# Kernel optimization log

Hardware: AMD Instinct MI355X
Metric: run time of the kernel (lower is better)

## Reference

```python
import jax, jax.numpy as jnp
import numpy as np

NEG = -1.0e30  # finite stand-in for -inf (NaN-safe under autodiff)


def rnnt_loss_mean(logits, ys, ylen):
    # logits: (B, T, U+1, V); ys: (B, U) int labels; ylen: (B,) label lengths.
    # blank index = 0; per the original forward, xlen == T for every batch element.
    lp = jax.nn.log_softmax(logits, axis=-1)
    lp_blank = lp[..., 0]  # (B, T, U1)
    # lp_label[b, t, u] = lp[b, t, u, ys[b, u]]  for u < U
    lp_label = jnp.take_along_axis(
        lp[:, :, :-1, :], ys[:, None, :, None].astype(jnp.int32), axis=3
    )[..., 0]  # (B, T, U)
    B, T, U1 = lp_blank.shape
    # emit[b, t, u] = lp_label[b, t, u-1], with emit[..., 0] = -inf
    emit = jnp.concatenate([jnp.full((B, T, 1), NEG, lp.dtype), lp_label], axis=2)
    # alpha[0, u] = sum_{k<u} lp_label[b, 0, k]
    row0 = jnp.concatenate(
        [jnp.zeros((B, 1), lp.dtype), jnp.cumsum(lp_label[:, 0, :], axis=1)], axis=1
    )  # (B, U1)

    def u_step(carry, au_eu):
        a_u, e_u = au_eu  # each (B,)
        new = jnp.logaddexp(a_u, carry + e_u)
        return new, new

    def t_step(prev_row, inp):
        blank_prev, emit_t = inp  # each (B, U1)
        a = prev_row + blank_prev  # horizontal (time) move
        init = jnp.full((B,), NEG, lp.dtype)
        _, new_row = jax.lax.scan(u_step, init, (a.T, emit_t.T))  # (U1, B)
        return new_row.T, None

    last_row, _ = jax.lax.scan(
        t_step,
        row0,
        (jnp.swapaxes(lp_blank[:, :-1, :], 0, 1), jnp.swapaxes(emit[:, 1:, :], 0, 1)),
    )  # (B, U1) = alpha[T-1, :]
    yl = ylen[:, None].astype(jnp.int32)
    alpha_end = jnp.take_along_axis(last_row, yl, axis=1)[:, 0]
    blank_end = jnp.take_along_axis(lp_blank[:, T - 1, :], yl, axis=1)[:, 0]
    return jnp.mean(-(alpha_end + blank_end))


def setup_inputs():
    B, T, U, H, V = 8, 200, 50, 320, 1024
    key = jax.random.key(0)
    ks = jax.random.split(key, 12)
    s = np.float32(1.0 / np.sqrt(H))
    return {
        "encoder_output": jax.random.normal(ks[0], (B, T, H), jnp.float32),
        "prediction_output": jax.random.normal(ks[1], (B, U + 1, H), jnp.float32),
        "xs": jax.random.normal(ks[2], (B, T, 80), jnp.float32),  # unused by forward
        "xlen": jnp.full((B,), T, jnp.int32),  # overwritten to T in original code
        "ys": jax.random.randint(ks[3], (B, U), 1, V, dtype=jnp.int32),
        "ylen": jax.random.randint(ks[4], (B,), 1, U + 1, dtype=jnp.int32),
        "W_enc": jax.random.normal(ks[5], (H, H), jnp.float32) * s,
        "b_enc": jnp.zeros((H,), jnp.float32),
        "W_pred": jax.random.normal(ks[6], (H, H), jnp.float32) * s,
        "b_pred": jnp.zeros((H,), jnp.float32),
        "W_ff_enc": jax.random.normal(ks[7], (H, V), jnp.float32) * s,
        "W_ff_pred": jax.random.normal(ks[8], (H, V), jnp.float32) * s,
        "b_ff": jnp.zeros((V,), jnp.float32),
    }


def reference(encoder_output, prediction_output, xs, xlen, ys, ylen,
              W_enc, b_enc, W_pred, b_pred, W_ff_enc, W_ff_pred, b_ff):
    # linear_enc / linear_pred commute with the broadcast-expand, so apply them first.
    enc_proj = encoder_output @ W_enc + b_enc        # (B, T, H)
    pred_proj = prediction_output @ W_pred + b_pred  # (B, U1, H)
    # cat + linear_feed_forward == split-weight matmuls summed over the broadcast.
    enc_part = enc_proj @ W_ff_enc    # (B, T, V)
    pred_part = pred_proj @ W_ff_pred  # (B, U1, V)
    logits = enc_part[:, :, None, :] + pred_part[:, None, :, :] + b_ff  # (B, T, U1, V)
    loss = rnnt_loss_mean(logits, ys, ylen)
    return loss, logits
```

## Files before the change

kernel.cpp:

```cpp
#include <hip/hip_runtime.h>
#include <hip/hip_bf16.h>
#include <cstddef>

#define Bdim 8
#define Tdim 200
#define Udim 50
#define U1dim 51
#define Hdim 320
#define Vdim 1024
#define NEGV -1.0e30f

using short8 = __attribute__((ext_vector_type(8))) short;
using f32x4  = __attribute__((ext_vector_type(4))) float;

static __device__ __forceinline__ ushort f2bf(float x) {
    __hip_bfloat16 h = __float2bfloat16(x);
    return *reinterpret_cast<ushort*>(&h);
}

__global__ __launch_bounds__(256) void cvt_bf16(
    const float* __restrict__ in, ushort* __restrict__ out, int n4)
{
    int i = blockIdx.x * 256 + threadIdx.x;
    if (i >= n4) return;
    float4 v = ((const float4*)in)[i];
    ushort4 o;
    o.x = f2bf(v.x); o.y = f2bf(v.y); o.z = f2bf(v.z); o.w = f2bf(v.w);
    ((ushort4*)out)[i] = o;
}

__global__ __launch_bounds__(256) void transpose_cvt(
    const float* __restrict__ W, ushort* __restrict__ Wt, int K, int N)
{
    __shared__ float tile[32][33];
    const int tx = threadIdx.x & 31, ty = threadIdx.x >> 5;
    const int n0 = blockIdx.x * 32, k0 = blockIdx.y * 32;
    #pragma unroll
    for (int i = 0; i < 4; ++i)
        tile[ty + i * 8][tx] = W[(size_t)(k0 + ty + i * 8) * N + n0 + tx];
    __syncthreads();
    #pragma unroll
    for (int i = 0; i < 4; ++i)
        Wt[(size_t)(n0 + ty + i * 8) * K + k0 + tx] = f2bf(tile[tx][ty + i * 8]);
}

template <bool OUT_BF16>
__global__ __launch_bounds__(256) void gemm_mfma(
    const ushort* __restrict__ A, const ushort* __restrict__ Bt,
    const float* __restrict__ bias, void* __restrict__ Cout,
    int M, int N, int K)
{
    __shared__ short As[64][40];
    __shared__ short Bs[64][40];
    const int tid = threadIdx.x;
    const int m0 = blockIdx.y * 64;
    const int n0 = blockIdx.x * 64;

    const int srow = tid >> 2;
    const int skc  = (tid & 3) * 8;

    const int lane = tid & 63;
    const int wave = tid >> 6;
    const int wr = wave >> 1, wc = wave & 1;
    const int lrow = lane & 15;
    const int kg = (lane >> 4) * 8;

    f32x4 acc[2][2] = {};

    for (int k0 = 0; k0 < K; k0 += 32) {
        int4 av = make_int4(0, 0, 0, 0);
        if (m0 + srow < M)
            av = *(const int4*)&A[(size_t)(m0 + srow) * K + k0 + skc];
        *(int4*)&As[srow][skc] = av;
        int4 bv = *(const int4*)&Bt[(size_t)(n0 + srow) * K + k0 + skc];
        *(int4*)&Bs[srow][skc] = bv;
        __syncthreads();

        short8 a0 = *(const short8*)&As[wr * 32 + lrow][kg];
        short8 a1 = *(const short8*)&As[wr * 32 + 16 + lrow][kg];
        short8 b0 = *(const short8*)&Bs[wc * 32 + lrow][kg];
        short8 b1 = *(const short8*)&Bs[wc * 32 + 16 + lrow][kg];
        acc[0][0] = __builtin_amdgcn_mfma_f32_16x16x32_bf16(a0, b0, acc[0][0], 0, 0, 0);
        acc[0][1] = __builtin_amdgcn_mfma_f32_16x16x32_bf16(a0, b1, acc[0][1], 0, 0, 0);
        acc[1][0] = __builtin_amdgcn_mfma_f32_16x16x32_bf16(a1, b0, acc[1][0], 0, 0, 0);
        acc[1][1] = __builtin_amdgcn_mfma_f32_16x16x32_bf16(a1, b1, acc[1][1], 0, 0, 0);
        __syncthreads();
    }

    #pragma unroll
    for (int fm = 0; fm < 2; ++fm) {
        #pragma unroll
        for (int fn = 0; fn < 2; ++fn) {
            int col = n0 + wc * 32 + fn * 16 + lrow;
            int r0 = m0 + wr * 32 + fm * 16 + (lane >> 4) * 4;
            float bv = bias ? bias[col] : 0.f;
            #pragma unroll
            for (int r = 0; r < 4; ++r) {
                int row = r0 + r;
                if (row < M) {
                    float val = acc[fm][fn][r] + bv;
                    if (OUT_BF16)
                        ((ushort*)Cout)[(size_t)row * N + col] = f2bf(val);
                    else
                        ((float*)Cout)[(size_t)row * N + col] = val;
                }
            }
        }
    }
}

__global__ __launch_bounds__(256) void joint_lse(
    const float* __restrict__ enc_part, const float* __restrict__ pred_part,
    const int* __restrict__ ys, float* __restrict__ out,
    float* __restrict__ lp_blank, float* __restrict__ lp_label)
{
    const int bt = blockIdx.x;
    const int b = bt / Tdim;
    const int tid = threadIdx.x;
    __shared__ float E[Vdim];
    *(float4*)&E[tid * 4] = *(const float4*)&enc_part[(size_t)bt * Vdim + tid * 4];
    __syncthreads();

    const int lane = tid & 63;
    const int wave = tid >> 6;
    float* logits = out + 1;

    for (int u = wave; u < U1dim; u += 4) {
        const float* P = pred_part + (size_t)(b * U1dim + u) * Vdim;
        float* Lrow = logits + ((size_t)bt * U1dim + u) * Vdim;
        float l[16];
        float m = -3.0e38f;
        #pragma unroll
        for (int k = 0; k < 16; ++k) {
            int v = k * 64 + lane;
            float x = E[v] + P[v];
            l[k] = x;
            Lrow[v] = x;
            m = fmaxf(m, x);
        }
        #pragma unroll
        for (int off = 32; off >= 1; off >>= 1) m = fmaxf(m, __shfl_xor(m, off));
        float s = 0.f;
        #pragma unroll
        for (int k = 0; k < 16; ++k) s += __expf(l[k] - m);
        #pragma unroll
        for (int off = 32; off >= 1; off >>= 1) s += __shfl_xor(s, off);
        float lse = m + __logf(s);

        int vlab = (u < Udim) ? ys[b * Udim + u] : 0;
        int ksel = vlab >> 6;
        int lsel = vlab & 63;
        float cand = 0.f;
        #pragma unroll
        for (int k = 0; k < 16; ++k) if (k == ksel) cand = l[k];
        float lab = __shfl(cand, lsel);
        float l0 = __shfl(l[0], 0);

        if (lane == 0) {
            lp_blank[(size_t)bt * U1dim + u] = l0 - lse;
            if (u < Udim) lp_label[(size_t)bt * Udim + u] = lab - lse;
        }
    }
}

__global__ __launch_bounds__(256) void alpha_kernel(
    const float* __restrict__ lp_blank, const float* __restrict__ lp_label,
    const int* __restrict__ ylen, float* __restrict__ loss_part)
{
    __shared__ float s_bl[U1dim * Tdim];
    __shared__ float s_lab[Udim * Tdim];
    const int b = blockIdx.x;
    const int tid = threadIdx.x;
    const float* gb = lp_blank + (size_t)b * Tdim * U1dim;
    const float* gl = lp_label + (size_t)b * Tdim * Udim;
    for (int i = tid; i < Tdim * U1dim; i += 256) {
        int t = i / U1dim, u = i % U1dim;
        s_bl[u * Tdim + t] = gb[i];
    }
    for (int i = tid; i < Tdim * Udim; i += 256) {
        int t = i / Udim, u = i % Udim;
        s_lab[u * Tdim + t] = gl[i];
    }
    __syncthreads();

    if (tid < 64) {
        const int u = tid;
        float cur = NEGV;
        for (int d = 0; d < Tdim + U1dim - 1; ++d) {
            float left = __shfl_up(cur, 1);
            int t = d - u;
            if (u < U1dim && t >= 0 && t < Tdim) {
                float h = (t >= 1) ? cur + s_bl[u * Tdim + (t - 1)] : NEGV;
                float g = (u >= 1) ? left + s_lab[(u - 1) * Tdim + t] : NEGV;
                float mx = fmaxf(h, g);
                float nv = mx + log1pf(__expf(-fabsf(h - g)));
                if (d == 0) nv = 0.f;
                cur = nv;
            }
        }
        const int L = ylen[b];
        if (u == L) loss_part[b] = -(cur + s_bl[L * Tdim + (Tdim - 1)]);
    }
}

__global__ void loss_mean(const float* __restrict__ loss_part, float* __restrict__ out)
{
    if (threadIdx.x == 0) {
        float s = 0.f;
        for (int i = 0; i < Bdim; ++i) s += loss_part[i];
        out[0] = s * (1.0f / Bdim);
    }
}

extern "C" void kernel_launch(void* const* d_in, const int* in_sizes, int n_in,
                              void* d_out, int out_size, void* d_ws, size_t ws_size,
                              hipStream_t stream)
{
    const float* enc      = (const float*)d_in[0];
    const float* pred     = (const float*)d_in[1];
    const int*   ys       = (const int*)d_in[4];
    const int*   ylen     = (const int*)d_in[5];
    const float* W_enc    = (const float*)d_in[6];
    const float* b_enc    = (const float*)d_in[7];
    const float* W_pred   = (const float*)d_in[8];
    const float* b_pred   = (const float*)d_in[9];
    const float* W_ff_enc = (const float*)d_in[10];
    const float* W_ff_pred= (const float*)d_in[11];
    const float* b_ff     = (const float*)d_in[12];
    float* out = (float*)d_out;
    char* ws = (char*)d_ws;

    ushort* enc_bf       = (ushort*)(ws + 0);
    ushort* pred_bf      = (ushort*)(ws + 1024000);
    float*  enc_part     = (float*) (ws + 0);
    float*  pred_part    = (float*) (ws + 6553600);
    float*  lp_blank     = (float*) (ws + 8224768);
    float*  lp_label     = (float*) (ws + 8551168);
    float*  loss_part    = (float*) (ws + 8871168);
    ushort* Wenc_t       = (ushort*)(ws + 8871200);
    ushort* Wpred_t      = (ushort*)(ws + 9076000);
    ushort* Wffe_t       = (ushort*)(ws + 9280800);
    ushort* Wffp_t       = (ushort*)(ws + 9936160);
    ushort* enc_proj_bf  = (ushort*)(ws + 10591520);
    ushort* pred_proj_bf = (ushort*)(ws + 11615520);

    dim3 blk(256);

    cvt_bf16<<<dim3(500), blk, 0, stream>>>(enc, enc_bf, 128000);
    cvt_bf16<<<dim3(128), blk, 0, stream>>>(pred, pred_bf, 32640);
    transpose_cvt<<<dim3(10, 10), blk, 0, stream>>>(W_enc,     Wenc_t, Hdim, Hdim);
    transpose_cvt<<<dim3(10, 10), blk, 0, stream>>>(W_pred,    Wpred_t, Hdim, Hdim);
    transpose_cvt<<<dim3(32, 10), blk, 0, stream>>>(W_ff_enc,  Wffe_t, Hdim, Vdim);
    transpose_cvt<<<dim3(32, 10), blk, 0, stream>>>(W_ff_pred, Wffp_t, Hdim, Vdim);

    gemm_mfma<true><<<dim3(5, 25), blk, 0, stream>>>(enc_bf, Wenc_t, b_enc, enc_proj_bf, Bdim * Tdim, Hdim, Hdim);
    gemm_mfma<true><<<dim3(5, 7), blk, 0, stream>>>(pred_bf, Wpred_t, b_pred, pred_proj_bf, Bdim * U1dim, Hdim, Hdim);
    gemm_mfma<false><<<dim3(16, 25), blk, 0, stream>>>(enc_proj_bf, Wffe_t, nullptr, enc_part, Bdim * Tdim, Vdim, Hdim);
    gemm_mfma<false><<<dim3(16, 7), blk, 0, stream>>>(pred_proj_bf, Wffp_t, b_ff, pred_part, Bdim * U1dim, Vdim, Hdim);

    joint_lse<<<dim3(Bdim * Tdim), blk, 0, stream>>>(enc_part, pred_part, ys, out, lp_blank, lp_label);
    alpha_kernel<<<dim3(Bdim), blk, 0, stream>>>(lp_blank, lp_label, ylen, loss_part);
    loss_mean<<<dim3(1), dim3(64), 0, stream>>>(loss_part, out);
}
```

Measured before the change: 243.9 us.

## Precompose projection weights and merge GEMMs, vectorize joint LSE, fold loss mean

The change multiplies W_ff by W_enc/W_pred once to form fused weights and bias vectors, turning two chained GEMMs per branch into one. Fp32 activations are converted to bf16 inside the GEMM load, which removes the separate convert and transpose kernels. Enc and pred GEMMs run in a single launch. joint_lse now loads contiguous float4 chunks per lane instead of going through shared memory, and the final mean becomes an atomicAdd in alpha_kernel. This cuts the launch count from thirteen to four and avoids intermediate buffers. In exchange, numerics change because the weights are precomposed in bf16, the float sum order becomes nondeterministic, and logits stores are unaligned because out is offset by one.

```diff
diff --git a/kernel.cpp b/kernel.cpp
--- a/kernel.cpp
+++ b/kernel.cpp
@@ -17,47 +17,54 @@
     __hip_bfloat16 h = __float2bfloat16(x);
     return *reinterpret_cast<ushort*>(&h);
 }
-
-__global__ __launch_bounds__(256) void cvt_bf16(
-    const float* __restrict__ in, ushort* __restrict__ out, int n4)
-{
-    int i = blockIdx.x * 256 + threadIdx.x;
-    if (i >= n4) return;
-    float4 v = ((const float4*)in)[i];
-    ushort4 o;
-    o.x = f2bf(v.x); o.y = f2bf(v.y); o.z = f2bf(v.z); o.w = f2bf(v.w);
-    ((ushort4*)out)[i] = o;
-}
-
-__global__ __launch_bounds__(256) void transpose_cvt(
-    const float* __restrict__ W, ushort* __restrict__ Wt, int K, int N)
-{
-    __shared__ float tile[32][33];
-    const int tx = threadIdx.x & 31, ty = threadIdx.x >> 5;
-    const int n0 = blockIdx.x * 32, k0 = blockIdx.y * 32;
-    #pragma unroll
-    for (int i = 0; i < 4; ++i)
-        tile[ty + i * 8][tx] = W[(size_t)(k0 + ty + i * 8) * N + n0 + tx];
-    __syncthreads();
-    #pragma unroll
-    for (int i = 0; i < 4; ++i)
-        Wt[(size_t)(n0 + ty + i * 8) * K + k0 + tx] = f2bf(tile[tx][ty + i * 8]);
-}
-
-template <bool OUT_BF16>
-__global__ __launch_bounds__(256) void gemm_mfma(
-    const ushort* __restrict__ A, const ushort* __restrict__ Bt,
-    const float* __restrict__ bias, void* __restrict__ Cout,
-    int M, int N, int K)
-{
+static __device__ __forceinline__ int pack2(float a, float b) {
+    return (int)f2bf(a) | ((int)f2bf(b) << 16);
+}
+
+__global__ __launch_bounds__(256) void fuse_weights(
+    const float* __restrict__ W_enc, const float* __restrict__ W_ff_enc,
+    const float* __restrict__ W_pred, const float* __restrict__ W_ff_pred,
+    const float* __restrict__ b_enc, const float* __restrict__ b_pred,
+    const float* __restrict__ b_ff,
+    ushort* __restrict__ Wfe_t, ushort* __restrict__ Wfp_t,
+    float* __restrict__ cvec, float* __restrict__ dvec)
+{
+    const int tid = threadIdx.x;
+    if (blockIdx.y == 16) {
+        if (blockIdx.x > 1) return;
+        const bool e = (blockIdx.x == 0);
+        const float* bv = e ? b_enc : b_pred;
+        const float* Wf = e ? W_ff_enc : W_ff_pred;
+        float* ovec = e ? cvec : dvec;
+        const int v = tid * 4;
+        float4 acc = make_float4(0.f, 0.f, 0.f, 0.f);
+        for (int p = 0; p < Hdim; ++p) {
+            float s = bv[p];
+            float4 w = *(const float4*)&Wf[(size_t)p * Vdim + v];
+            acc.x += s * w.x; acc.y += s * w.y; acc.z += s * w.z; acc.w += s * w.w;
+        }
+        if (e) {
+            float4 bf = *(const float4*)&b_ff[v];
+            acc.x += bf.x; acc.y += bf.y; acc.z += bf.z; acc.w += bf.w;
+        }
+        *(float4*)&ovec[v] = acc;
+        return;
+    }
+
+    const bool e = (blockIdx.x < 5);
+    const float* A  = e ? W_ff_enc : W_ff_pred;
+    const float* Bm = e ? W_enc    : W_pred;
+    ushort* Cout    = e ? Wfe_t    : Wfp_t;
+    const int n0 = (blockIdx.x % 5) * 64;
+    const int m0 = blockIdx.y * 64;
+
     __shared__ short As[64][40];
     __shared__ short Bs[64][40];
-    const int tid = threadIdx.x;
-    const int m0 = blockIdx.y * 64;
-    const int n0 = blockIdx.x * 64;
-
-    const int srow = tid >> 2;
-    const int skc  = (tid & 3) * 8;
+
+    const int ar = tid >> 3;
+    const int ac = (tid & 7) * 8;
+    const int br = tid >> 2;
+    const int bc = (tid & 3) * 8;
 
     const int lane = tid & 63;
     const int wave = tid >> 6;
@@ -67,23 +74,32 @@
 
     f32x4 acc[2][2] = {};
 
-    for (int k0 = 0; k0 < K; k0 += 32) {
-        int4 av = make_int4(0, 0, 0, 0);
-        if (m0 + srow < M)
-            av = *(const int4*)&A[(size_t)(m0 + srow) * K + k0 + skc];
-        *(int4*)&As[srow][skc] = av;
-        int4 bv = *(const int4*)&Bt[(size_t)(n0 + srow) * K + k0 + skc];
-        *(int4*)&Bs[srow][skc] = bv;
+    for (int k0 = 0; k0 < Hdim; k0 += 32) {
+        float4 a0 = *(const float4*)&A[(size_t)(k0 + ar) * Vdim + m0 + ac];
+        float4 a1 = *(const float4*)&A[(size_t)(k0 + ar) * Vdim + m0 + ac + 4];
+        As[ac + 0][ar] = (short)f2bf(a0.x);
+        As[ac + 1][ar] = (short)f2bf(a0.y);
+        As[ac + 2][ar] = (short)f2bf(a0.z);
+        As[ac + 3][ar] = (short)f2bf(a0.w);
+        As[ac + 4][ar] = (short)f2bf(a1.x);
+        As[ac + 5][ar] = (short)f2bf(a1.y);
+        As[ac + 6][ar] = (short)f2bf(a1.z);
+        As[ac + 7][ar] = (short)f2bf(a1.w);
+        float4 w0 = *(const float4*)&Bm[(size_t)(n0 + br) * Hdim + k0 + bc];
+        float4 w1 = *(const float4*)&Bm[(size_t)(n0 + br) * Hdim + k0 + bc + 4];
+        int4 bp = make_int4(pack2(w0.x, w0.y), pack2(w0.z, w0.w),
+                            pack2(w1.x, w1.y), pack2(w1.z, w1.w));
+        *(int4*)&Bs[br][bc] = bp;
         __syncthreads();
 
-        short8 a0 = *(const short8*)&As[wr * 32 + lrow][kg];
-        short8 a1 = *(const short8*)&As[wr * 32 + 16 + lrow][kg];
-        short8 b0 = *(const short8*)&Bs[wc * 32 + lrow][kg];
-        short8 b1 = *(const short8*)&Bs[wc * 32 + 16 + lrow][kg];
-        acc[0][0] = __builtin_amdgcn_mfma_f32_16x16x32_bf16(a0, b0, acc[0][0], 0, 0, 0);
-        acc[0][1] = __builtin_amdgcn_mfma_f32_16x16x32_bf16(a0, b1, acc[0][1], 0, 0, 0);
-        acc[1][0] = __builtin_amdgcn_mfma_f32_16x16x32_bf16(a1, b0, acc[1][0], 0, 0, 0);
-        acc[1][1] = __builtin_amdgcn_mfma_f32_16x16x32_bf16(a1, b1, acc[1][1], 0, 0, 0);
+        short8 fa0 = *(const short8*)&As[wr * 32 + lrow][kg];
+        short8 fa1 = *(const short8*)&As[wr * 32 + 16 + lrow][kg];
+        short8 fb0 = *(const short8*)&Bs[wc * 32 + lrow][kg];
+        short8 fb1 = *(const short8*)&Bs[wc * 32 + 16 + lrow][kg];
+        acc[0][0] = __builtin_amdgcn_mfma_f32_16x16x32_bf16(fa0, fb0, acc[0][0], 0, 0, 0);
+        acc[0][1] = __builtin_amdgcn_mfma_f32_16x16x32_bf16(fa0, fb1, acc[0][1], 0, 0, 0);
+        acc[1][0] = __builtin_amdgcn_mfma_f32_16x16x32_bf16(fa1, fb0, acc[1][0], 0, 0, 0);
+        acc[1][1] = __builtin_amdgcn_mfma_f32_16x16x32_bf16(fa1, fb1, acc[1][1], 0, 0, 0);
         __syncthreads();
     }
 
@@ -93,17 +109,77 @@
         for (int fn = 0; fn < 2; ++fn) {
             int col = n0 + wc * 32 + fn * 16 + lrow;
             int r0 = m0 + wr * 32 + fm * 16 + (lane >> 4) * 4;
-            float bv = bias ? bias[col] : 0.f;
+            #pragma unroll
+            for (int r = 0; r < 4; ++r)
+                Cout[(size_t)(r0 + r) * Hdim + col] = f2bf(acc[fm][fn][r]);
+        }
+    }
+}
+
+__global__ __launch_bounds__(256) void main_gemm(
+    const float* __restrict__ enc, const float* __restrict__ pred,
+    const ushort* __restrict__ Wfe_t, const ushort* __restrict__ Wfp_t,
+    const float* __restrict__ cvec, const float* __restrict__ dvec,
+    float* __restrict__ enc_part, float* __restrict__ pred_part)
+{
+    const bool e = (blockIdx.y < 25);
+    const float*  A    = e ? enc : pred;
+    const ushort* Bt   = e ? Wfe_t : Wfp_t;
+    const float*  bias = e ? cvec : dvec;
+    float*        C    = e ? enc_part : pred_part;
+    const int M  = e ? (Bdim * Tdim) : (Bdim * U1dim);
+    const int m0 = (e ? blockIdx.y : blockIdx.y - 25) * 64;
+    const int n0 = blockIdx.x * 64;
+
+    __shared__ short As[64][40];
+    __shared__ short Bs[64][40];
+    const int tid = threadIdx.x;
+    const int sr = tid >> 2;
+    const int sc = (tid & 3) * 8;
+
+    const int lane = tid & 63;
+    const int wave = tid >> 6;
+    const int wr = wave >> 1, wc = wave & 1;
+    const int lrow = lane & 15;
+    const int kg = (lane >> 4) * 8;
+
+    f32x4 acc[2][2] = {};
+
+    for (int k0 = 0; k0 < Hdim; k0 += 32) {
+        int4 av = make_int4(0, 0, 0, 0);
+        if (m0 + sr < M) {
+            float4 x0 = *(const float4*)&A[(size_t)(m0 + sr) * Hdim + k0 + sc];
+            float4 x1 = *(const float4*)&A[(size_t)(m0 + sr) * Hdim + k0 + sc + 4];
+            av = make_int4(pack2(x0.x, x0.y), pack2(x0.z, x0.w),
+                           pack2(x1.x, x1.y), pack2(x1.z, x1.w));
+        }
+        *(int4*)&As[sr][sc] = av;
+        *(int4*)&Bs[sr][sc] = *(const int4*)&Bt[(size_t)(n0 + sr) * Hdim + k0 + sc];
+        __syncthreads();
+
+        short8 fa0 = *(const short8*)&As[wr * 32 + lrow][kg];
+        short8 fa1 = *(const short8*)&As[wr * 32 + 16 + lrow][kg];
+        short8 fb0 = *(const short8*)&Bs[wc * 32 + lrow][kg];
+        short8 fb1 = *(const short8*)&Bs[wc * 32 + 16 + lrow][kg];
+        acc[0][0] = __builtin_amdgcn_mfma_f32_16x16x32_bf16(fa0, fb0, acc[0][0], 0, 0, 0);
+        acc[0][1] = __builtin_amdgcn_mfma_f32_16x16x32_bf16(fa0, fb1, acc[0][1], 0, 0, 0);
+        acc[1][0] = __builtin_amdgcn_mfma_f32_16x16x32_bf16(fa1, fb0, acc[1][0], 0, 0, 0);
+        acc[1][1] = __builtin_amdgcn_mfma_f32_16x16x32_bf16(fa1, fb1, acc[1][1], 0, 0, 0);
+        __syncthreads();
+    }
+
+    #pragma unroll
+    for (int fm = 0; fm < 2; ++fm) {
+        #pragma unroll
+        for (int fn = 0; fn < 2; ++fn) {
+            int col = n0 + wc * 32 + fn * 16 + lrow;
+            int r0 = m0 + wr * 32 + fm * 16 + (lane >> 4) * 4;
+            float bv = bias[col];
             #pragma unroll
             for (int r = 0; r < 4; ++r) {
                 int row = r0 + r;
-                if (row < M) {
-                    float val = acc[fm][fn][r] + bv;
-                    if (OUT_BF16)
-                        ((ushort*)Cout)[(size_t)row * N + col] = f2bf(val);
-                    else
-                        ((float*)Cout)[(size_t)row * N + col] = val;
-                }
+                if (row < M)
+                    C[(size_t)row * Vdim + col] = acc[fm][fn][r] + bv;
             }
         }
     }
@@ -117,44 +193,57 @@
     const int bt = blockIdx.x;
     const int b = bt / Tdim;
     const int tid = threadIdx.x;
-    __shared__ float E[Vdim];
-    *(float4*)&E[tid * 4] = *(const float4*)&enc_part[(size_t)bt * Vdim + tid * 4];
-    __syncthreads();
-
     const int lane = tid & 63;
     const int wave = tid >> 6;
+    if (bt == 0 && tid == 0) out[0] = 0.f;
+
+    const float* Erow = enc_part + (size_t)bt * Vdim + lane * 16;
+    float4 e0 = *(const float4*)(Erow + 0);
+    float4 e1 = *(const float4*)(Erow + 4);
+    float4 e2 = *(const float4*)(Erow + 8);
+    float4 e3 = *(const float4*)(Erow + 12);
+
     float* logits = out + 1;
 
     for (int u = wave; u < U1dim; u += 4) {
-        const float* P = pred_part + (size_t)(b * U1dim + u) * Vdim;
-        float* Lrow = logits + ((size_t)bt * U1dim + u) * Vdim;
-        float l[16];
-        float m = -3.0e38f;
-        #pragma unroll
-        for (int k = 0; k < 16; ++k) {
-            int v = k * 64 + lane;
-            float x = E[v] + P[v];
-            l[k] = x;
-            Lrow[v] = x;
-            m = fmaxf(m, x);
-        }
+        const float* P = pred_part + (size_t)(b * U1dim + u) * Vdim + lane * 16;
+        float4 p0 = *(const float4*)(P + 0);
+        float4 p1 = *(const float4*)(P + 4);
+        float4 p2 = *(const float4*)(P + 8);
+        float4 p3 = *(const float4*)(P + 12);
+        float xa[16];
+        xa[0]=e0.x+p0.x;  xa[1]=e0.y+p0.y;  xa[2]=e0.z+p0.z;  xa[3]=e0.w+p0.w;
+        xa[4]=e1.x+p1.x;  xa[5]=e1.y+p1.y;  xa[6]=e1.z+p1.z;  xa[7]=e1.w+p1.w;
+        xa[8]=e2.x+p2.x;  xa[9]=e2.y+p2.y;  xa[10]=e2.z+p2.z; xa[11]=e2.w+p2.w;
+        xa[12]=e3.x+p3.x; xa[13]=e3.y+p3.y; xa[14]=e3.z+p3.z; xa[15]=e3.w+p3.w;
+
+        float* L = logits + (size_t)bt * U1dim * Vdim + (size_t)u * Vdim + lane * 16;
+        L[0] = xa[0]; L[1] = xa[1]; L[2] = xa[2];
+        *(float4*)(L + 3)  = make_float4(xa[3],  xa[4],  xa[5],  xa[6]);
+        *(float4*)(L + 7)  = make_float4(xa[7],  xa[8],  xa[9],  xa[10]);
+        *(float4*)(L + 11) = make_float4(xa[11], xa[12], xa[13], xa[14]);
+        L[15] = xa[15];
+
+        float m = xa[0];
+        #pragma unroll
+        for (int i = 1; i < 16; ++i) m = fmaxf(m, xa[i]);
         #pragma unroll
         for (int off = 32; off >= 1; off >>= 1) m = fmaxf(m, __shfl_xor(m, off));
         float s = 0.f;
         #pragma unroll
-        for (int k = 0; k < 16; ++k) s += __expf(l[k] - m);
+        for (int i = 0; i < 16; ++i) s += __expf(xa[i] - m);
         #pragma unroll
         for (int off = 32; off >= 1; off >>= 1) s += __shfl_xor(s, off);
         float lse = m + __logf(s);
 
         int vlab = (u < Udim) ? ys[b * Udim + u] : 0;
-        int ksel = vlab >> 6;
-        int lsel = vlab & 63;
-        float cand = 0.f;
-        #pragma unroll
-        for (int k = 0; k < 16; ++k) if (k == ksel) cand = l[k];
-        float lab = __shfl(cand, lsel);
-        float l0 = __shfl(l[0], 0);
+        int idx = vlab & 15;
+        int src = vlab >> 4;
+        float cand = xa[0];
+        #pragma unroll
+        for (int i = 1; i < 16; ++i) if (i == idx) cand = xa[i];
+        float lab = __shfl(cand, src);
+        float l0 = __shfl(xa[0], 0);
 
         if (lane == 0) {
             lp_blank[(size_t)bt * U1dim + u] = l0 - lse;
@@ -165,7 +254,7 @@
 
 __global__ __launch_bounds__(256) void alpha_kernel(
     const float* __restrict__ lp_blank, const float* __restrict__ lp_label,
-    const int* __restrict__ ylen, float* __restrict__ loss_part)
+    const int* __restrict__ ylen, float* __restrict__ out)
 {
     __shared__ float s_bl[U1dim * Tdim];
     __shared__ float s_lab[Udim * Tdim];
@@ -199,16 +288,8 @@
             }
         }
         const int L = ylen[b];
-        if (u == L) loss_part[b] = -(cur + s_bl[L * Tdim + (Tdim - 1)]);
-    }
-}
-
-__global__ void loss_mean(const float* __restrict__ loss_part, float* __restrict__ out)
-{
-    if (threadIdx.x == 0) {
-        float s = 0.f;
-        for (int i = 0; i < Bdim; ++i) s += loss_part[i];
-        out[0] = s * (1.0f / Bdim);
+        if (u == L)
+            atomicAdd(out, -(cur + s_bl[L * Tdim + (Tdim - 1)]) * (1.0f / Bdim));
     }
 }
 
@@ -230,35 +311,22 @@
     float* out = (float*)d_out;
     char* ws = (char*)d_ws;
 
-    ushort* enc_bf       = (ushort*)(ws + 0);
-    ushort* pred_bf      = (ushort*)(ws + 1024000);
-    float*  enc_part     = (float*) (ws + 0);
-    float*  pred_part    = (float*) (ws + 6553600);
-    float*  lp_blank     = (float*) (ws + 8224768);
-    float*  lp_label     = (float*) (ws + 8551168);
-    float*  loss_part    = (float*) (ws + 8871168);
-    ushort* Wenc_t       = (ushort*)(ws + 8871200);
-    ushort* Wpred_t      = (ushort*)(ws + 9076000);
-    ushort* Wffe_t       = (ushort*)(ws + 9280800);
-    ushort* Wffp_t       = (ushort*)(ws + 9936160);
-    ushort* enc_proj_bf  = (ushort*)(ws + 10591520);
-    ushort* pred_proj_bf = (ushort*)(ws + 11615520);
+    float*  enc_part  = (float*) (ws + 0);
+    float*  pred_part = (float*) (ws + 6553600);
+    ushort* Wfe_t     = (ushort*)(ws + 8224768);
+    ushort* Wfp_t     = (ushort*)(ws + 8880128);
+    float*  cvec      = (float*) (ws + 9535488);
+    float*  dvec      = (float*) (ws + 9539584);
+    float*  lp_blank  = (float*) (ws + 9543680);
+    float*  lp_label  = (float*) (ws + 9870080);
 
     dim3 blk(256);
-
-    cvt_bf16<<<dim3(500), blk, 0, stream>>>(enc, enc_bf, 128000);
-    cvt_bf16<<<dim3(128), blk, 0, stream>>>(pred, pred_bf, 32640);
-    transpose_cvt<<<dim3(10, 10), blk, 0, stream>>>(W_enc,     Wenc_t, Hdim, Hdim);
-    transpose_cvt<<<dim3(10, 10), blk, 0, stream>>>(W_pred,    Wpred_t, Hdim, Hdim);
-    transpose_cvt<<<dim3(32, 10), blk, 0, stream>>>(W_ff_enc,  Wffe_t, Hdim, Vdim);
-    transpose_cvt<<<dim3(32, 10), blk, 0, stream>>>(W_ff_pred, Wffp_t, Hdim, Vdim);
-
-    gemm_mfma<true><<<dim3(5, 25), blk, 0, stream>>>(enc_bf, Wenc_t, b_enc, enc_proj_bf, Bdim * Tdim, Hdim, Hdim);
-    gemm_mfma<true><<<dim3(5, 7), blk, 0, stream>>>(pred_bf, Wpred_t, b_pred, pred_proj_bf, Bdim * U1dim, Hdim, Hdim);
-    gemm_mfma<false><<<dim3(16, 25), blk, 0, stream>>>(enc_proj_bf, Wffe_t, nullptr, enc_part, Bdim * Tdim, Vdim, Hdim);
-    gemm_mfma<false><<<dim3(16, 7), blk, 0, stream>>>(pred_proj_bf, Wffp_t, b_ff, pred_part, Bdim * U1dim, Vdim, Hdim);
-
-    joint_lse<<<dim3(Bdim * Tdim), blk, 0, stream>>>(enc_part, pred_part, ys, out, lp_blank, lp_label);
-    alpha_kernel<<<dim3(Bdim), blk, 0, stream>>>(lp_blank, lp_label, ylen, loss_part);
-    loss_mean<<<dim3(1), dim3(64), 0, stream>>>(loss_part, out);
-}
+    fuse_weights<<<dim3(10, 17), blk, 0, stream>>>(
+        W_enc, W_ff_enc, W_pred, W_ff_pred, b_enc, b_pred, b_ff,
+        Wfe_t, Wfp_t, cvec, dvec);
+    main_gemm<<<dim3(16, 32), blk, 0, stream>>>(
+        enc, pred, Wfe_t, Wfp_t, cvec, dvec, enc_part, pred_part);
+    joint_lse<<<dim3(Bdim * Tdim), blk, 0, stream>>>(
+        enc_part, pred_part, ys, out, lp_blank, lp_label);
+    alpha_kernel<<<dim3(Bdim), blk, 0, stream>>>(lp_blank, lp_label, ylen, out);
+}
```

After: 246.0 us. No clear change (+0.9%).
